# Optimization experiments

Measured on AMD Instinct MI355X. Metric: run time of the kernel, lower is better.

## Reference

```python
import jax, jax.numpy as jnp
import numpy as np

D = 128
NUM_STRUCTURES = 8
N = 1024
BERNOULLI_INIT = 0.5


def setup_inputs() -> dict:
    key = jax.random.key(0)
    k_x, k_m, k_w = jax.random.split(key, 3)
    x = jax.random.normal(k_x, (N, D), dtype=jnp.float32)
    # maskings: 0/1 DAG masks (one per structure), float for multiplication
    maskings = jax.random.randint(k_m, (NUM_STRUCTURES, D, D), 0, 2).astype(jnp.float32)
    # Bernoulli logits/probs theta, initialized at bernouilli_init
    theta = jnp.full((NUM_STRUCTURES, D, D), BERNOULLI_INIT, dtype=jnp.float32)
    # Linear structural-equation weights
    W = jax.random.normal(k_w, (NUM_STRUCTURES, D, D), dtype=jnp.float32)
    return {"x": x, "maskings": maskings, "theta": theta, "W": W}


def _bernoulli_ste(theta):
    # BernoulliSTERoot: hard Bernoulli sample with straight-through estimator.
    # Fixed noise key for deterministic reference.
    u = jax.random.uniform(jax.random.key(42), theta.shape, dtype=theta.dtype)
    hard = (u < theta).astype(theta.dtype)
    return theta + jax.lax.stop_gradient(hard - theta)


def reference(x, maskings, theta, W):
    # dags[o,p,c]: masked Bernoulli sample of edge p->c for structure o
    dags = maskings * _bernoulli_ste(theta)  # (o, d, d)
    # masked_x[o,n,c,p] = dags[o,p,c] * x[n,p]  (large 4-D intermediate, as in original)
    masked_x = jnp.einsum('opc,np->oncp', dags, x)  # (o, n, d, d)
    # x_hat[o,n,c] = sum_p masked_x[o,n,c,p] * W[o,p,c]
    x_hat = jnp.einsum('oncp,opc->onc', masked_x, W)  # (o, n, d)
    return x_hat
```

## Files before the change

### kernel.cpp

```cpp
#include <hip/hip_runtime.h>
#include <stdint.h>

#define NSTRUCT 8
#define NROWS   1024
#define DD      128

typedef short bf16x8 __attribute__((ext_vector_type(8)));
typedef float f32x4  __attribute__((ext_vector_type(4)));

__device__ __forceinline__ uint32_t rotl32(uint32_t x, uint32_t d) {
  return (x << d) | (x >> (32u - d));
}

__device__ __forceinline__ uint32_t threefry_bits(uint32_t i) {
  const uint32_t ks0 = 0u;
  const uint32_t ks1 = 42u;
  const uint32_t ks2 = 0x1BD11BDAu ^ ks0 ^ ks1;
  uint32_t x0 = 0u + ks0;
  uint32_t x1 = i  + ks1;
#define TF_RND(r) { x0 += x1; x1 = rotl32(x1, r); x1 ^= x0; }
  TF_RND(13) TF_RND(15) TF_RND(26) TF_RND(6)
  x0 += ks1; x1 += ks2 + 1u;
  TF_RND(17) TF_RND(29) TF_RND(16) TF_RND(24)
  x0 += ks2; x1 += ks0 + 2u;
  TF_RND(13) TF_RND(15) TF_RND(26) TF_RND(6)
  x0 += ks0; x1 += ks1 + 3u;
  TF_RND(17) TF_RND(29) TF_RND(16) TF_RND(24)
  x0 += ks1; x1 += ks2 + 4u;
  TF_RND(13) TF_RND(15) TF_RND(26) TF_RND(6)
  x0 += ks2; x1 += ks0 + 5u;
#undef TF_RND
  return x0 ^ x1;
}

__device__ __forceinline__ uint16_t f32_to_bf16_rne(float v) {
  uint32_t fb = __float_as_uint(v);
  uint32_t lsb = (fb >> 16) & 1u;
  return (uint16_t)((fb + 0x7fffu + lsb) >> 16);
}

__global__ __launch_bounds__(256) void build_frags(
    const float* __restrict__ x,
    const float* __restrict__ maskings,
    const float* __restrict__ theta,
    const float* __restrict__ W,
    uint16_t* __restrict__ Mb,
    uint16_t* __restrict__ xb) {
  const int b = blockIdx.x;
  const int tid = threadIdx.x;
  if (b < 512) {
    uint32_t flat = (uint32_t)b * 256u + tid;
    uint32_t j    = flat & 7u;
    uint32_t lane = (flat >> 3) & 63u;
    uint32_t kk   = (flat >> 9) & 3u;
    uint32_t ct   = (flat >> 11) & 7u;
    uint32_t o    = flat >> 14;
    uint32_t p = kk * 32u + (lane >> 4) * 8u + j;
    uint32_t c = ct * 16u + (lane & 15u);
    uint32_t gi = (o << 14) | (p << 7) | c;
    uint32_t bits = threefry_bits(gi);
    float u = __uint_as_float((bits >> 9) | 0x3f800000u) - 1.0f;
    float v = (u < theta[gi]) ? maskings[gi] * W[gi] : 0.0f;
    Mb[flat] = f32_to_bf16_rne(v);
  } else {
    uint32_t idx  = (uint32_t)(b - 512) * 256u + tid;
    uint32_t j    = idx & 7u;
    uint32_t lane = (idx >> 3) & 63u;
    uint32_t kk   = (idx >> 9) & 3u;
    uint32_t rt   = idx >> 11;
    uint32_t n = rt * 16u + (lane & 15u);
    uint32_t k = kk * 32u + (lane >> 4) * 8u + j;
    xb[idx] = f32_to_bf16_rne(x[n * DD + k]);
  }
}

__global__ __launch_bounds__(256) void sem_mfma(
    const uint16_t* __restrict__ Mb,
    const uint16_t* __restrict__ xb,
    float* __restrict__ out) {
  const int bidx = blockIdx.x;
  const int o    = bidx >> 5;
  const int rb   = bidx & 31;
  const int tid  = threadIdx.x;
  const int w    = tid >> 6;
  const int lane = tid & 63;
  const int rt_g = rb * 2 + (w & 1);
  const int ctb  = (w >> 1) * 4;

  const bf16x8* xbv = (const bf16x8*)xb;
  const bf16x8* mbv = (const bf16x8*)Mb;

  bf16x8 a[4];
#pragma unroll
  for (int kk = 0; kk < 4; ++kk) a[kk] = xbv[(rt_g * 4 + kk) * 64 + lane];

  f32x4 acc[4] = {{0.f, 0.f, 0.f, 0.f}, {0.f, 0.f, 0.f, 0.f},
                  {0.f, 0.f, 0.f, 0.f}, {0.f, 0.f, 0.f, 0.f}};

#pragma unroll
  for (int t = 0; t < 4; ++t) {
    const int ct = ctb + t;
#pragma unroll
    for (int kk = 0; kk < 4; ++kk) {
      bf16x8 bfrag = mbv[((o * 8 + ct) * 4 + kk) * 64 + lane];
      acc[t] = __builtin_amdgcn_mfma_f32_16x16x32_bf16(a[kk], bfrag, acc[t], 0, 0, 0);
    }
  }

  const int col0     = lane & 15;
  const int row_base = rb * 32 + (w & 1) * 16 + (lane >> 4) * 4;
#pragma unroll
  for (int t = 0; t < 4; ++t) {
    const int col = (ctb + t) * 16 + col0;
#pragma unroll
    for (int r = 0; r < 4; ++r) {
      out[((size_t)o * NROWS + row_base + r) * DD + col] = acc[t][r];
    }
  }
}


extern "C" void kernel_launch(void* const* d_in, const int* in_sizes, int n_in,
                              void* d_out, int out_size, void* d_ws, size_t ws_size,
                              hipStream_t stream) {
  const float* x        = (const float*)d_in[0];
  const float* maskings = (const float*)d_in[1];
  const float* theta    = (const float*)d_in[2];
  const float* W        = (const float*)d_in[3];
  float* out = (float*)d_out;

  uint16_t* Mb = (uint16_t*)d_ws;
  uint16_t* xb = Mb + NSTRUCT * DD * DD;

  build_frags<<<1024, 256, 0, stream>>>(x, maskings, theta, W, Mb, xb);
  sem_mfma<<<NSTRUCT * 32, 256, 0, stream>>>(Mb, xb, out);
}
```

Measured before the change: 63.18 us.

## Fuse mask generation and bf16 MFMA into one kernel using LDS fragments

Merges the fragment-building kernel and the MFMA kernel into a single launch. Each block builds one 16-column slice of the masked weight matrix in shared memory and converts x to bf16 in registers before the MFMA calls. This removes the second launch and the workspace round trip through global memory. In exchange, each block recomputes its slice (threefry per element, redundant across the 8 row-quarter blocks) and converts x on the fly, reading x repeatedly.

```diff
diff --git a/kernel.cpp b/kernel.cpp
--- a/kernel.cpp
+++ b/kernel.cpp
@@ -39,82 +39,78 @@
   return (uint16_t)((fb + 0x7fffu + lsb) >> 16);
 }
 
-__global__ __launch_bounds__(256) void build_frags(
+__global__ __launch_bounds__(256) void sem_fused(
     const float* __restrict__ x,
     const float* __restrict__ maskings,
     const float* __restrict__ theta,
     const float* __restrict__ W,
-    uint16_t* __restrict__ Mb,
-    uint16_t* __restrict__ xb) {
-  const int b = blockIdx.x;
+    float* __restrict__ out) {
+  __shared__ uint16_t Mlds[4 * 64 * 8];
+
+  const int b  = blockIdx.x;
+  const int cs = b & 7;
+  const int rq = (b >> 3) & 7;
+  const int o  = b >> 6;
   const int tid = threadIdx.x;
-  if (b < 512) {
-    uint32_t flat = (uint32_t)b * 256u + tid;
-    uint32_t j    = flat & 7u;
-    uint32_t lane = (flat >> 3) & 63u;
-    uint32_t kk   = (flat >> 9) & 3u;
-    uint32_t ct   = (flat >> 11) & 7u;
-    uint32_t o    = flat >> 14;
-    uint32_t p = kk * 32u + (lane >> 4) * 8u + j;
-    uint32_t c = ct * 16u + (lane & 15u);
-    uint32_t gi = (o << 14) | (p << 7) | c;
-    uint32_t bits = threefry_bits(gi);
-    float u = __uint_as_float((bits >> 9) | 0x3f800000u) - 1.0f;
-    float v = (u < theta[gi]) ? maskings[gi] * W[gi] : 0.0f;
-    Mb[flat] = f32_to_bf16_rne(v);
-  } else {
-    uint32_t idx  = (uint32_t)(b - 512) * 256u + tid;
-    uint32_t j    = idx & 7u;
-    uint32_t lane = (idx >> 3) & 63u;
-    uint32_t kk   = (idx >> 9) & 3u;
-    uint32_t rt   = idx >> 11;
-    uint32_t n = rt * 16u + (lane & 15u);
-    uint32_t k = kk * 32u + (lane >> 4) * 8u + j;
-    xb[idx] = f32_to_bf16_rne(x[n * DD + k]);
+
+  {
+    const int c  = tid & 15;
+    const int pb = tid >> 4;
+    const int cg = cs * 16 + c;
+#pragma unroll
+    for (int i = 0; i < 8; ++i) {
+      const int p = pb + i * 16;
+      const uint32_t gi = ((uint32_t)o << 14) | ((uint32_t)p << 7) | (uint32_t)cg;
+      const uint32_t bits = threefry_bits(gi);
+      const float u = __uint_as_float((bits >> 9) | 0x3f800000u) - 1.0f;
+      const float v = (u < theta[gi]) ? maskings[gi] * W[gi] : 0.0f;
+      const int idx = (((p >> 5) * 64) + ((((p >> 3) & 3) << 4) | c)) * 8 + (p & 7);
+      Mlds[idx] = f32_to_bf16_rne(v);
+    }
   }
-}
+  __syncthreads();
 
-__global__ __launch_bounds__(256) void sem_mfma(
-    const uint16_t* __restrict__ Mb,
-    const uint16_t* __restrict__ xb,
-    float* __restrict__ out) {
-  const int bidx = blockIdx.x;
-  const int o    = bidx >> 5;
-  const int rb   = bidx & 31;
-  const int tid  = threadIdx.x;
   const int w    = tid >> 6;
   const int lane = tid & 63;
-  const int rt_g = rb * 2 + (w & 1);
-  const int ctb  = (w >> 1) * 4;
 
-  const bf16x8* xbv = (const bf16x8*)xb;
-  const bf16x8* mbv = (const bf16x8*)Mb;
+  const bf16x8* mf = (const bf16x8*)Mlds;
+  bf16x8 bfrag[4];
+#pragma unroll
+  for (int kk = 0; kk < 4; ++kk) bfrag[kk] = mf[kk * 64 + lane];
 
-  bf16x8 a[4];
+  f32x4 acc[2] = {{0.f, 0.f, 0.f, 0.f}, {0.f, 0.f, 0.f, 0.f}};
+
+  const int arow = lane & 15;
+  const int k0   = (lane >> 4) * 8;
 #pragma unroll
-  for (int kk = 0; kk < 4; ++kk) a[kk] = xbv[(rt_g * 4 + kk) * 64 + lane];
-
-  f32x4 acc[4] = {{0.f, 0.f, 0.f, 0.f}, {0.f, 0.f, 0.f, 0.f},
-                  {0.f, 0.f, 0.f, 0.f}, {0.f, 0.f, 0.f, 0.f}};
-
-#pragma unroll
-  for (int t = 0; t < 4; ++t) {
-    const int ct = ctb + t;
+  for (int m = 0; m < 2; ++m) {
+    const int rt  = rq * 8 + w * 2 + m;
+    const float* xp = x + (rt * 16 + arow) * DD + k0;
 #pragma unroll
     for (int kk = 0; kk < 4; ++kk) {
-      bf16x8 bfrag = mbv[((o * 8 + ct) * 4 + kk) * 64 + lane];
-      acc[t] = __builtin_amdgcn_mfma_f32_16x16x32_bf16(a[kk], bfrag, acc[t], 0, 0, 0);
+      const float4 lo = *(const float4*)(xp + kk * 32);
+      const float4 hi = *(const float4*)(xp + kk * 32 + 4);
+      bf16x8 a;
+      a[0] = (short)f32_to_bf16_rne(lo.x);
+      a[1] = (short)f32_to_bf16_rne(lo.y);
+      a[2] = (short)f32_to_bf16_rne(lo.z);
+      a[3] = (short)f32_to_bf16_rne(lo.w);
+      a[4] = (short)f32_to_bf16_rne(hi.x);
+      a[5] = (short)f32_to_bf16_rne(hi.y);
+      a[6] = (short)f32_to_bf16_rne(hi.z);
+      a[7] = (short)f32_to_bf16_rne(hi.w);
+      acc[m] = __builtin_amdgcn_mfma_f32_16x16x32_bf16(a, bfrag[kk], acc[m], 0, 0, 0);
     }
   }
 
-  const int col0     = lane & 15;
-  const int row_base = rb * 32 + (w & 1) * 16 + (lane >> 4) * 4;
+  const int col   = cs * 16 + (lane & 15);
+  const int rbase = (lane >> 4) * 4;
 #pragma unroll
-  for (int t = 0; t < 4; ++t) {
-    const int col = (ctb + t) * 16 + col0;
+  for (int m = 0; m < 2; ++m) {
+    const int rt = rq * 8 + w * 2 + m;
 #pragma unroll
     for (int r = 0; r < 4; ++r) {
-      out[((size_t)o * NROWS + row_base + r) * DD + col] = acc[t][r];
+      out[((size_t)o * NROWS + rt * 16 + rbase + r) * DD + col] = acc[m][r];
     }
   }
 }
@@ -123,15 +119,12 @@
 extern "C" void kernel_launch(void* const* d_in, const int* in_sizes, int n_in,
                               void* d_out, int out_size, void* d_ws, size_t ws_size,
                               hipStream_t stream) {
+  (void)in_sizes; (void)n_in; (void)out_size; (void)d_ws; (void)ws_size;
   const float* x        = (const float*)d_in[0];
   const float* maskings = (const float*)d_in[1];
   const float* theta    = (const float*)d_in[2];
   const float* W        = (const float*)d_in[3];
   float* out = (float*)d_out;
 
-  uint16_t* Mb = (uint16_t*)d_ws;
-  uint16_t* xb = Mb + NSTRUCT * DD * DD;
-
-  build_frags<<<1024, 256, 0, stream>>>(x, maskings, theta, W, Mb, xb);
-  sem_mfma<<<NSTRUCT * 32, 256, 0, stream>>>(Mb, xb, out);
+  sem_fused<<<NSTRUCT * 8 * 8, 256, 0, stream>>>(x, maskings, theta, W, out);
 }
```

Measured after the change: 67.67 us. 7.1% more time.
